# Performance work log

Measured on AMD Instinct MI355X. Metric: run time of the kernel, lower is better.

## Reference

```python
import jax, jax.numpy as jnp
import numpy as np

EMBED_DIM = 1024
NUM_HEADS = 16
HEAD_DIM = EMBED_DIM // NUM_HEADS
ROPE_BASE = 10000.0


def _rope_cos_sin(seq_len, head_dim, dtype):
    # Standard RoPE (ESM-style rotate_half): freqs outer(t, inv_freq), emb = cat(freqs, freqs)
    inv_freq = 1.0 / (ROPE_BASE ** (jnp.arange(0, head_dim, 2, dtype=jnp.float32) / head_dim))
    t = jnp.arange(seq_len, dtype=jnp.float32)
    freqs = jnp.einsum('s,d->sd', t, inv_freq)          # [s, d/2]
    emb = jnp.concatenate([freqs, freqs], axis=-1)      # [s, d]
    return jnp.cos(emb).astype(dtype), jnp.sin(emb).astype(dtype)


def _rotate_half(x):
    x1, x2 = jnp.split(x, 2, axis=-1)
    return jnp.concatenate([-x2, x1], axis=-1)


def _apply_rope(x, cos, sin):
    # x: [b, h, s, d]; cos/sin: [s, d] broadcast over b, h
    return x * cos + _rotate_half(x) * sin


def setup_inputs() -> dict:
    key = jax.random.key(0)
    ks = jax.random.split(key, 5)
    b, s, e = 4, 2048, EMBED_DIM
    scale = 1.0 / np.sqrt(e)
    x = jax.random.normal(ks[0], (b, s, e), dtype=jnp.float32)
    Wqkv = jax.random.normal(ks[1], (e, 3 * e), dtype=jnp.float32) * scale
    bqkv = jnp.zeros((3 * e,), dtype=jnp.float32)
    Wo = jax.random.normal(ks[2], (e, e), dtype=jnp.float32) * scale
    bo = jnp.zeros((e,), dtype=jnp.float32)
    return {"x": x, "Wqkv": Wqkv, "bqkv": bqkv, "Wo": Wo, "bo": bo}


def reference(x, Wqkv, bqkv, Wo, bo):
    b, s, e = x.shape
    h, d = NUM_HEADS, HEAD_DIM
    qkv = jnp.einsum('bse,ef->bsf', x, Wqkv) + bqkv          # [b, s, 3e]
    q, k, v = jnp.split(qkv, 3, axis=-1)
    # b s (h d) -> b h s d
    q = q.reshape(b, s, h, d).transpose(0, 2, 1, 3)
    k = k.reshape(b, s, h, d).transpose(0, 2, 1, 3)
    v = v.reshape(b, s, h, d).transpose(0, 2, 1, 3)
    cos, sin = _rope_cos_sin(s, d, x.dtype)
    q = _apply_rope(q, cos, sin)
    k = _apply_rope(k, cos, sin)
    # scaled dot product attention (no mask, no dropout, non-causal)
    scores = jnp.einsum('bhqd,bhkd->bhqk', q, k) / jnp.asarray(np.sqrt(d), x.dtype)
    attn = jax.nn.softmax(scores, axis=-1)
    out = jnp.einsum('bhqk,bhkd->bhqd', attn, v)             # [b, h, s, d]
    out = out.transpose(0, 2, 1, 3).reshape(b, s, e)         # b h s d -> b s (h d)
    return jnp.einsum('bse,ef->bsf', out, Wo) + bo
```

## Files before the change

kernel.cpp:

```cpp
#include <hip/hip_runtime.h>
#include <stdint.h>
#include <stddef.h>

typedef __bf16 bf16;
typedef __attribute__((ext_vector_type(8))) __bf16 bf16x8;
typedef __attribute__((ext_vector_type(4))) __bf16 bf16x4;
typedef __attribute__((ext_vector_type(4))) float f32x4;
typedef __attribute__((ext_vector_type(4))) float float4v;

#define BATCH 4
#define SEQ   2048
#define EMB   1024
#define NH    16
#define HD    64
#define F3    3072

#define MFMA16(a, b, c) __builtin_amdgcn_mfma_f32_16x16x32_bf16((a), (b), (c), 0, 0, 0)

__device__ __forceinline__ void gload_lds16(const bf16* g, bf16* l) {
  __builtin_amdgcn_global_load_lds(
      (const __attribute__((address_space(1))) uint32_t*)g,
      (__attribute__((address_space(3))) uint32_t*)l, 16, 0, 0);
}

__global__ __launch_bounds__(256) void rope_table(float* __restrict__ cosT,
                                                  float* __restrict__ sinT) {
  int idx = blockIdx.x * 256 + threadIdx.x;
  int pos = idx >> 5, d1 = idx & 31;
  float inv = powf(10000.0f, -(float)(2 * d1) / 64.0f);
  float th = (float)pos * inv;
  cosT[idx] = cosf(th);
  sinT[idx] = sinf(th);
}

__global__ __launch_bounds__(256) void convert_bf16(const float* __restrict__ src,
                                                    bf16* __restrict__ dst, int n4) {
  int i = blockIdx.x * 256 + threadIdx.x;
  if (i >= n4) return;
  float4v v = ((const float4v*)src)[i];
  bf16x4 o;
#pragma unroll
  for (int k = 0; k < 4; ++k) o[k] = (bf16)v[k];
  ((bf16x4*)dst)[i] = o;
}

__global__ __launch_bounds__(256) void transpose_f32_bf16(const float* __restrict__ in,
                                                          bf16* __restrict__ out,
                                                          int R, int C) {
  __shared__ bf16 tile[32][33];
  const int tx = threadIdx.x & 31;
  const int ty = threadIdx.x >> 5;
  const int c0 = blockIdx.x * 32, r0 = blockIdx.y * 32;
#pragma unroll
  for (int kk = 0; kk < 4; ++kk) {
    int r = ty + kk * 8;
    tile[r][tx] = (bf16)in[(size_t)(r0 + r) * C + c0 + tx];
  }
  __syncthreads();
#pragma unroll
  for (int kk = 0; kk < 4; ++kk) {
    int r = ty + kk * 8;
    out[(size_t)(c0 + r) * R + r0 + tx] = tile[tx][r];
  }
}

__global__ __launch_bounds__(256) void qkv_rope_kernel(
    const bf16* __restrict__ x, const bf16* __restrict__ wT,
    const float* __restrict__ bias, bf16* __restrict__ qo, bf16* __restrict__ ko,
    bf16* __restrict__ vo, const float* __restrict__ cosT,
    const float* __restrict__ sinT) {
  __shared__ __align__(16) bf16 As[128 * 32];
  __shared__ __align__(16) bf16 Bs[128 * 32];
  const int tid = threadIdx.x;
  const int w = tid >> 6, lane = tid & 63;
  const int lhi = lane >> 4, llo = lane & 15;
  const int wr = w >> 1, wc = w & 1;
  const int row_a0 = blockIdx.y * 128;
  const int row_b0 = blockIdx.x * 128;

  f32x4 acc[4][4];
#pragma unroll
  for (int i = 0; i < 4; ++i)
#pragma unroll
    for (int j = 0; j < 4; ++j) acc[i][j] = (f32x4){0.f, 0.f, 0.f, 0.f};

  for (int k0 = 0; k0 < EMB; k0 += 32) {
#pragma unroll
    for (int c = 0; c < 2; ++c) {
      int chunk = w * 2 + c;
      int gl = chunk * 64 + lane;
      int row = gl >> 2, kk = (gl & 3) << 3;
      gload_lds16(x + (size_t)(row_a0 + row) * EMB + k0 + kk, &As[chunk * 512]);
      gload_lds16(wT + (size_t)(row_b0 + row) * EMB + k0 + kk, &Bs[chunk * 512]);
    }
    __syncthreads();
    bf16x8 a[4], b[4];
#pragma unroll
    for (int i = 0; i < 4; ++i)
      a[i] = *(const bf16x8*)&As[(wr * 64 + i * 16 + llo) * 32 + lhi * 8];
#pragma unroll
    for (int j = 0; j < 4; ++j)
      b[j] = *(const bf16x8*)&Bs[(wc * 64 + j * 16 + llo) * 32 + lhi * 8];
#pragma unroll
    for (int i = 0; i < 4; ++i)
#pragma unroll
      for (int j = 0; j < 4; ++j) acc[i][j] = MFMA16(a[i], b[j], acc[i][j]);
    __syncthreads();
  }

  const int f0 = row_b0 + wc * 64;
  const int part = f0 >> 10;
  const int hh = (f0 & 1023) >> 6;
  const int m_base = row_a0 + wr * 64;

  float bvals[4];
#pragma unroll
  for (int j = 0; j < 4; ++j) bvals[j] = bias[f0 + j * 16 + llo];

  if (part == 2) {
#pragma unroll
    for (int i = 0; i < 4; ++i) {
      int m0 = m_base + i * 16 + lhi * 4;
      int bb = m0 >> 11, pos0 = m0 & 2047;
#pragma unroll
      for (int j = 0; j < 4; ++j) {
        int dd = j * 16 + llo;
        bf16x4 pk;
#pragma unroll
        for (int r = 0; r < 4; ++r) pk[r] = (bf16)(acc[i][j][r] + bvals[j]);
        *(bf16x4*)(vo + ((size_t)(bb * NH + hh) * HD + dd) * SEQ + pos0) = pk;
      }
    }
  } else {
    bf16* dst = (part == 0) ? qo : ko;
    const float qs = (part == 0) ? 0.125f : 1.0f;
#pragma unroll
    for (int i = 0; i < 4; ++i) {
#pragma unroll
      for (int r = 0; r < 4; ++r) {
        int m = m_base + i * 16 + lhi * 4 + r;
        int bb = m >> 11, pos = m & 2047;
        size_t base = ((size_t)(bb * NH + hh) * SEQ + pos) * HD;
#pragma unroll
        for (int j = 0; j < 2; ++j) {
          int d1 = j * 16 + llo;
          float x1 = acc[i][j][r] + bvals[j];
          float x2 = acc[i][j + 2][r] + bvals[j + 2];
          float cth = cosT[pos * 32 + d1];
          float sth = sinT[pos * 32 + d1];
          dst[base + d1] = (bf16)((x1 * cth - x2 * sth) * qs);
          dst[base + d1 + 32] = (bf16)((x2 * cth + x1 * sth) * qs);
        }
      }
    }
  }
}

__global__ __launch_bounds__(256) void attn_kernel(const bf16* __restrict__ q,
                                                   const bf16* __restrict__ k,
                                                   const bf16* __restrict__ vT,
                                                   bf16* __restrict__ o) {
  __shared__ __align__(16) bf16 smem[24576];
  bf16* Qs = smem;

  const int tid = threadIdx.x, w = tid >> 6, lane = tid & 63;
  const int lhi = lane >> 4, llo = lane & 15;
  const int l7 = llo & 7;
  const int bidx = blockIdx.x;
  const int vblk = (bidx & 7) * 128 + (bidx >> 3);
  const int qt = vblk & 15, bh = vblk >> 4;
  const bf16* qbase = q + (size_t)bh * SEQ * HD + qt * 128 * HD;
  const bf16* kbase = k + (size_t)bh * SEQ * HD;
  const bf16* vbase = vT + (size_t)bh * HD * SEQ;
  bf16* Pw = smem + w * 2048;

  const int rowc = lane >> 3;
  const int sw8 = (lane & 7) ^ rowc;

#pragma unroll
  for (int c = 0; c < 4; ++c) {
    int chunk = w * 4 + c;
    int row = chunk * 8 + rowc;
    gload_lds16(qbase + (size_t)row * HD + sw8 * 8, &Qs[chunk * 512]);
  }
#pragma unroll
  for (int c = 0; c < 2; ++c) {
    int chunk = w * 2 + c;
    int row = chunk * 8 + rowc;
    gload_lds16(kbase + (size_t)row * HD + sw8 * 8, &smem[8192 + chunk * 512]);
    gload_lds16(vbase + (size_t)row * SEQ + sw8 * 8, &smem[16384 + chunk * 512]);
  }
  __syncthreads();

  bf16x8 qf[2][2];
#pragma unroll
  for (int i = 0; i < 2; ++i)
#pragma unroll
    for (int kc = 0; kc < 2; ++kc)
      qf[i][kc] = *(const bf16x8*)&Qs[(w * 32 + i * 16 + llo) * 64 +
                                      (((kc * 4 + lhi) ^ l7) * 8)];
  __syncthreads();

  float rsum[2][4];
  f32x4 oacc[2][4];
#pragma unroll
  for (int i = 0; i < 2; ++i)
#pragma unroll
    for (int r = 0; r < 4; ++r) rsum[i][r] = 0.f;
#pragma unroll
  for (int i = 0; i < 2; ++i)
#pragma unroll
    for (int j = 0; j < 4; ++j) oacc[i][j] = (f32x4){0.f, 0.f, 0.f, 0.f};

  for (int kb = 0; kb < 32; ++kb) {
    bf16* Kc = smem + 8192 + (kb & 1) * 4096;
    bf16* Vc = smem + 16384 + (kb & 1) * 4096;
    if (kb < 31) {
      bf16* Kn = smem + 8192 + ((kb + 1) & 1) * 4096;
      bf16* Vn = smem + 16384 + ((kb + 1) & 1) * 4096;
      int kpos = (kb + 1) * 64;
#pragma unroll
      for (int c = 0; c < 2; ++c) {
        int chunk = w * 2 + c;
        int row = chunk * 8 + rowc;
        gload_lds16(kbase + (size_t)(kpos + row) * HD + sw8 * 8, &Kn[chunk * 512]);
        gload_lds16(vbase + (size_t)row * SEQ + kpos + sw8 * 8, &Vn[chunk * 512]);
      }
    }
    f32x4 sacc[2][4];
#pragma unroll
    for (int i = 0; i < 2; ++i)
#pragma unroll
      for (int jn = 0; jn < 4; ++jn) sacc[i][jn] = (f32x4){0.f, 0.f, 0.f, 0.f};
#pragma unroll
    for (int kc = 0; kc < 2; ++kc) {
      bf16x8 bfr[4];
#pragma unroll
      for (int jn = 0; jn < 4; ++jn)
        bfr[jn] = *(const bf16x8*)&Kc[(jn * 16 + llo) * 64 +
                                      (((kc * 4 + lhi) ^ l7) * 8)];
#pragma unroll
      for (int i = 0; i < 2; ++i)
#pragma unroll
        for (int jn = 0; jn < 4; ++jn)
          sacc[i][jn] = MFMA16(qf[i][kc], bfr[jn], sacc[i][jn]);
    }
#pragma unroll
    for (int i = 0; i < 2; ++i) {
#pragma unroll
      for (int r = 0; r < 4; ++r) {
        int qrow = i * 16 + lhi * 4 + r;
        int qb = qrow * 64, q7 = qrow & 7;
        float acc = 0.f;
#pragma unroll
        for (int jn = 0; jn < 4; ++jn) {
          float p = __expf(sacc[i][jn][r]);
          Pw[qb + (((jn * 2 + (llo >> 3)) ^ q7) * 8) + l7] = (bf16)p;
          acc += p;
        }
        rsum[i][r] += acc;
      }
    }
#pragma unroll
    for (int kc = 0; kc < 2; ++kc) {
      bf16x8 af[2], bv[4];
      int xg = ((kc * 4 + lhi) ^ l7) * 8;
#pragma unroll
      for (int i = 0; i < 2; ++i)
        af[i] = *(const bf16x8*)&Pw[(i * 16 + llo) * 64 + xg];
#pragma unroll
      for (int jd = 0; jd < 4; ++jd)
        bv[jd] = *(const bf16x8*)&Vc[(jd * 16 + llo) * 64 + xg];
#pragma unroll
      for (int i = 0; i < 2; ++i)
#pragma unroll
        for (int jd = 0; jd < 4; ++jd) oacc[i][jd] = MFMA16(af[i], bv[jd], oacc[i][jd]);
    }
    __syncthreads();
  }

  const int bb = bh >> 4, hh = bh & 15;
#pragma unroll
  for (int i = 0; i < 2; ++i) {
#pragma unroll
    for (int r = 0; r < 4; ++r) {
      float t = rsum[i][r];
      t += __shfl_xor(t, 1);
      t += __shfl_xor(t, 2);
      t += __shfl_xor(t, 4);
      t += __shfl_xor(t, 8);
      float inv = 1.0f / t;
      int pos = qt * 128 + w * 32 + i * 16 + lhi * 4 + r;
      size_t base = ((size_t)bb * SEQ + pos) * EMB + hh * HD;
#pragma unroll
      for (int jd = 0; jd < 4; ++jd)
        o[base + jd * 16 + llo] = (bf16)(oacc[i][jd][r] * inv);
    }
  }
}

__global__ __launch_bounds__(256) void outproj_kernel(const bf16* __restrict__ a_in,
                                                      const bf16* __restrict__ wT,
                                                      const float* __restrict__ bo,
                                                      float* __restrict__ out) {
  __shared__ __align__(16) bf16 As[128 * 32];
  __shared__ __align__(16) bf16 Bs[128 * 32];
  const int tid = threadIdx.x;
  const int w = tid >> 6, lane = tid & 63;
  const int lhi = lane >> 4, llo = lane & 15;
  const int wr = w >> 1, wc = w & 1;
  const int row_a0 = blockIdx.y * 128;
  const int row_b0 = blockIdx.x * 128;

  f32x4 acc[4][4];
#pragma unroll
  for (int i = 0; i < 4; ++i)
#pragma unroll
    for (int j = 0; j < 4; ++j) acc[i][j] = (f32x4){0.f, 0.f, 0.f, 0.f};

  for (int k0 = 0; k0 < EMB; k0 += 32) {
#pragma unroll
    for (int c = 0; c < 2; ++c) {
      int chunk = w * 2 + c;
      int gl = chunk * 64 + lane;
      int row = gl >> 2, kk = (gl & 3) << 3;
      gload_lds16(a_in + (size_t)(row_a0 + row) * EMB + k0 + kk, &As[chunk * 512]);
      gload_lds16(wT + (size_t)(row_b0 + row) * EMB + k0 + kk, &Bs[chunk * 512]);
    }
    __syncthreads();
    bf16x8 a[4], b[4];
#pragma unroll
    for (int i = 0; i < 4; ++i)
      a[i] = *(const bf16x8*)&As[(wr * 64 + i * 16 + llo) * 32 + lhi * 8];
#pragma unroll
    for (int j = 0; j < 4; ++j)
      b[j] = *(const bf16x8*)&Bs[(wc * 64 + j * 16 + llo) * 32 + lhi * 8];
#pragma unroll
    for (int i = 0; i < 4; ++i)
#pragma unroll
      for (int j = 0; j < 4; ++j) acc[i][j] = MFMA16(a[i], b[j], acc[i][j]);
    __syncthreads();
  }

  const int col0 = row_b0 + wc * 64;
  const int m_base = row_a0 + wr * 64;
  float bvals[4];
#pragma unroll
  for (int j = 0; j < 4; ++j) bvals[j] = bo[col0 + j * 16 + llo];
#pragma unroll
  for (int i = 0; i < 4; ++i) {
#pragma unroll
    for (int r = 0; r < 4; ++r) {
      int m = m_base + i * 16 + lhi * 4 + r;
#pragma unroll
      for (int j = 0; j < 4; ++j)
        out[(size_t)m * EMB + col0 + j * 16 + llo] = acc[i][j][r] + bvals[j];
    }
  }
}

extern "C" void kernel_launch(void* const* d_in, const int* in_sizes, int n_in,
                              void* d_out, int out_size, void* d_ws, size_t ws_size,
                              hipStream_t stream) {
  const float* x_raw = (const float*)d_in[0];
  const float* wqkv_raw = (const float*)d_in[1];
  const float* bqkv = (const float*)d_in[2];
  const float* wo_raw = (const float*)d_in[3];
  const float* bo = (const float*)d_in[4];
  float* out = (float*)d_out;

  char* ws = (char*)d_ws;
  bf16* qw = (bf16*)(ws);
  bf16* kw = (bf16*)(ws + 16777216);
  bf16* vw = (bf16*)(ws + 33554432);
  bf16* wqkvT = (bf16*)(ws + 50331648);
  float* cosT = (float*)(ws + 56623104);
  float* sinT = (float*)(ws + 56885248);
  bf16* ow = (bf16*)(ws + 50331648);
  bf16* woT = (bf16*)(ws);
  bf16* xb = (bf16*)d_out;

  rope_table<<<256, 256, 0, stream>>>(cosT, sinT);
  convert_bf16<<<(BATCH * SEQ * EMB / 4 + 255) / 256, 256, 0, stream>>>(
      x_raw, xb, BATCH * SEQ * EMB / 4);
  transpose_f32_bf16<<<dim3(F3 / 32, EMB / 32), 256, 0, stream>>>(wqkv_raw, wqkvT, EMB, F3);

  qkv_rope_kernel<<<dim3(F3 / 128, (BATCH * SEQ) / 128), 256, 0, stream>>>(
      xb, wqkvT, bqkv, qw, kw, vw, cosT, sinT);
  attn_kernel<<<dim3(BATCH * NH * (SEQ / 128)), 256, 0, stream>>>(qw, kw, vw, ow);

  transpose_f32_bf16<<<dim3(EMB / 32, EMB / 32), 256, 0, stream>>>(wo_raw, woT, EMB, EMB);
  outproj_kernel<<<dim3(EMB / 128, (BATCH * SEQ) / 128), 256, 0, stream>>>(
      ow, woT, bo, out);
}
```

Before: 309.0 us.

## Widen attention blocks to 256 queries, split K/V loads, transpose score MFMA

The attention kernel now uses 512 threads (8 waves) covering 256 query rows per block, so each K/V tile staged in LDS is shared by twice as many query rows, halving K/V global traffic. Waves 0-3 load K and waves 4-7 load V instead of every wave loading both. The score MFMA is computed as K·Q^T, so each lane holds four consecutive keys for one query. P is then written as packed bf16x4 stores, and the row sum reduces with two shuffles plus a broadcast. The trade-offs are a larger LDS footprint (64 KB per block) and half as many blocks, which may lower occupancy and tail utilisation.

```diff
diff --git a/kernel.cpp b/kernel.cpp
--- a/kernel.cpp
+++ b/kernel.cpp
@@ -156,20 +156,20 @@
   }
 }
 
-__global__ __launch_bounds__(256) void attn_kernel(const bf16* __restrict__ q,
+__global__ __launch_bounds__(512) void attn_kernel(const bf16* __restrict__ q,
                                                    const bf16* __restrict__ k,
                                                    const bf16* __restrict__ vT,
                                                    bf16* __restrict__ o) {
-  __shared__ __align__(16) bf16 smem[24576];
+  __shared__ __align__(16) bf16 smem[32768];
   bf16* Qs = smem;
 
   const int tid = threadIdx.x, w = tid >> 6, lane = tid & 63;
   const int lhi = lane >> 4, llo = lane & 15;
   const int l7 = llo & 7;
   const int bidx = blockIdx.x;
-  const int vblk = (bidx & 7) * 128 + (bidx >> 3);
-  const int qt = vblk & 15, bh = vblk >> 4;
-  const bf16* qbase = q + (size_t)bh * SEQ * HD + qt * 128 * HD;
+  const int vblk = (bidx & 7) * 64 + (bidx >> 3);
+  const int qt = vblk & 7, bh = vblk >> 3;
+  const bf16* qbase = q + (size_t)bh * SEQ * HD + qt * 256 * HD;
   const bf16* kbase = k + (size_t)bh * SEQ * HD;
   const bf16* vbase = vT + (size_t)bh * HD * SEQ;
   bf16* Pw = smem + w * 2048;
@@ -183,12 +183,20 @@
     int row = chunk * 8 + rowc;
     gload_lds16(qbase + (size_t)row * HD + sw8 * 8, &Qs[chunk * 512]);
   }
-#pragma unroll
-  for (int c = 0; c < 2; ++c) {
-    int chunk = w * 2 + c;
-    int row = chunk * 8 + rowc;
-    gload_lds16(kbase + (size_t)row * HD + sw8 * 8, &smem[8192 + chunk * 512]);
-    gload_lds16(vbase + (size_t)row * SEQ + sw8 * 8, &smem[16384 + chunk * 512]);
+  if (w < 4) {
+#pragma unroll
+    for (int c = 0; c < 2; ++c) {
+      int chunk = w * 2 + c;
+      int row = chunk * 8 + rowc;
+      gload_lds16(kbase + (size_t)row * HD + sw8 * 8, &smem[16384 + chunk * 512]);
+    }
+  } else {
+#pragma unroll
+    for (int c = 0; c < 2; ++c) {
+      int chunk = (w - 4) * 2 + c;
+      int row = chunk * 8 + rowc;
+      gload_lds16(vbase + (size_t)row * SEQ + sw8 * 8, &smem[24576 + chunk * 512]);
+    }
   }
   __syncthreads();
 
@@ -201,73 +209,79 @@
                                       (((kc * 4 + lhi) ^ l7) * 8)];
   __syncthreads();
 
-  float rsum[2][4];
+  float rsum[2] = {0.f, 0.f};
   f32x4 oacc[2][4];
 #pragma unroll
   for (int i = 0; i < 2; ++i)
 #pragma unroll
-    for (int r = 0; r < 4; ++r) rsum[i][r] = 0.f;
-#pragma unroll
-  for (int i = 0; i < 2; ++i)
-#pragma unroll
     for (int j = 0; j < 4; ++j) oacc[i][j] = (f32x4){0.f, 0.f, 0.f, 0.f};
 
   for (int kb = 0; kb < 32; ++kb) {
-    bf16* Kc = smem + 8192 + (kb & 1) * 4096;
-    bf16* Vc = smem + 16384 + (kb & 1) * 4096;
+    bf16* Kc = smem + 16384 + (kb & 1) * 4096;
+    bf16* Vc = smem + 24576 + (kb & 1) * 4096;
     if (kb < 31) {
-      bf16* Kn = smem + 8192 + ((kb + 1) & 1) * 4096;
-      bf16* Vn = smem + 16384 + ((kb + 1) & 1) * 4096;
       int kpos = (kb + 1) * 64;
-#pragma unroll
-      for (int c = 0; c < 2; ++c) {
-        int chunk = w * 2 + c;
-        int row = chunk * 8 + rowc;
-        gload_lds16(kbase + (size_t)(kpos + row) * HD + sw8 * 8, &Kn[chunk * 512]);
-        gload_lds16(vbase + (size_t)row * SEQ + kpos + sw8 * 8, &Vn[chunk * 512]);
+      if (w < 4) {
+        bf16* Kn = smem + 16384 + ((kb + 1) & 1) * 4096;
+#pragma unroll
+        for (int c = 0; c < 2; ++c) {
+          int chunk = w * 2 + c;
+          int row = chunk * 8 + rowc;
+          gload_lds16(kbase + (size_t)(kpos + row) * HD + sw8 * 8, &Kn[chunk * 512]);
+        }
+      } else {
+        bf16* Vn = smem + 24576 + ((kb + 1) & 1) * 4096;
+#pragma unroll
+        for (int c = 0; c < 2; ++c) {
+          int chunk = (w - 4) * 2 + c;
+          int row = chunk * 8 + rowc;
+          gload_lds16(vbase + (size_t)row * SEQ + kpos + sw8 * 8, &Vn[chunk * 512]);
+        }
       }
     }
-    f32x4 sacc[2][4];
-#pragma unroll
-    for (int i = 0; i < 2; ++i)
-#pragma unroll
-      for (int jn = 0; jn < 4; ++jn) sacc[i][jn] = (f32x4){0.f, 0.f, 0.f, 0.f};
+    f32x4 st[4][2];
+#pragma unroll
+    for (int tt = 0; tt < 4; ++tt)
+#pragma unroll
+      for (int i = 0; i < 2; ++i) st[tt][i] = (f32x4){0.f, 0.f, 0.f, 0.f};
 #pragma unroll
     for (int kc = 0; kc < 2; ++kc) {
-      bf16x8 bfr[4];
-#pragma unroll
-      for (int jn = 0; jn < 4; ++jn)
-        bfr[jn] = *(const bf16x8*)&Kc[(jn * 16 + llo) * 64 +
+      bf16x8 kfr[4];
+#pragma unroll
+      for (int tt = 0; tt < 4; ++tt)
+        kfr[tt] = *(const bf16x8*)&Kc[(tt * 16 + llo) * 64 +
                                       (((kc * 4 + lhi) ^ l7) * 8)];
 #pragma unroll
-      for (int i = 0; i < 2; ++i)
-#pragma unroll
-        for (int jn = 0; jn < 4; ++jn)
-          sacc[i][jn] = MFMA16(qf[i][kc], bfr[jn], sacc[i][jn]);
-    }
-#pragma unroll
-    for (int i = 0; i < 2; ++i) {
-#pragma unroll
-      for (int r = 0; r < 4; ++r) {
-        int qrow = i * 16 + lhi * 4 + r;
-        int qb = qrow * 64, q7 = qrow & 7;
-        float acc = 0.f;
-#pragma unroll
-        for (int jn = 0; jn < 4; ++jn) {
-          float p = __expf(sacc[i][jn][r]);
-          Pw[qb + (((jn * 2 + (llo >> 3)) ^ q7) * 8) + l7] = (bf16)p;
-          acc += p;
+      for (int tt = 0; tt < 4; ++tt)
+#pragma unroll
+        for (int i = 0; i < 2; ++i)
+          st[tt][i] = MFMA16(kfr[tt], qf[i][kc], st[tt][i]);
+    }
+#pragma unroll
+    for (int tt = 0; tt < 4; ++tt) {
+#pragma unroll
+      for (int i = 0; i < 2; ++i) {
+        bf16x4 pk;
+        float a = 0.f;
+#pragma unroll
+        for (int r = 0; r < 4; ++r) {
+          float p = __expf(st[tt][i][r]);
+          pk[r] = (bf16)p;
+          a += p;
         }
-        rsum[i][r] += acc;
+        rsum[i] += a;
+        int gi = (tt * 4 + lhi) ^ (l7 << 1);
+        *(bf16x4*)&Pw[(i * 16 + llo) * 64 + gi * 4] = pk;
       }
     }
 #pragma unroll
     for (int kc = 0; kc < 2; ++kc) {
       bf16x8 af[2], bv[4];
       int xg = ((kc * 4 + lhi) ^ l7) * 8;
+      int pg = ((kc * 8 + lhi * 2) ^ (l7 << 1)) * 4;
 #pragma unroll
       for (int i = 0; i < 2; ++i)
-        af[i] = *(const bf16x8*)&Pw[(i * 16 + llo) * 64 + xg];
+        af[i] = *(const bf16x8*)&Pw[(i * 16 + llo) * 64 + pg];
 #pragma unroll
       for (int jd = 0; jd < 4; ++jd)
         bv[jd] = *(const bf16x8*)&Vc[(jd * 16 + llo) * 64 + xg];
@@ -282,15 +296,14 @@
   const int bb = bh >> 4, hh = bh & 15;
 #pragma unroll
   for (int i = 0; i < 2; ++i) {
+    float t = rsum[i];
+    t += __shfl_xor(t, 16);
+    t += __shfl_xor(t, 32);
 #pragma unroll
     for (int r = 0; r < 4; ++r) {
-      float t = rsum[i][r];
-      t += __shfl_xor(t, 1);
-      t += __shfl_xor(t, 2);
-      t += __shfl_xor(t, 4);
-      t += __shfl_xor(t, 8);
-      float inv = 1.0f / t;
-      int pos = qt * 128 + w * 32 + i * 16 + lhi * 4 + r;
+      float l = __shfl(t, lhi * 4 + r);
+      float inv = 1.0f / l;
+      int pos = qt * 256 + w * 32 + i * 16 + lhi * 4 + r;
       size_t base = ((size_t)bb * SEQ + pos) * EMB + hh * HD;
 #pragma unroll
       for (int jd = 0; jd < 4; ++jd)
@@ -387,7 +400,7 @@
 
   qkv_rope_kernel<<<dim3(F3 / 128, (BATCH * SEQ) / 128), 256, 0, stream>>>(
       xb, wqkvT, bqkv, qw, kw, vw, cosT, sinT);
-  attn_kernel<<<dim3(BATCH * NH * (SEQ / 128)), 256, 0, stream>>>(qw, kw, vw, ow);
+  attn_kernel<<<dim3(BATCH * NH * (SEQ / 256)), 512, 0, stream>>>(qw, kw, vw, ow);
 
   transpose_f32_bf16<<<dim3(EMB / 32, EMB / 32), 256, 0, stream>>>(wo_raw, woT, EMB, EMB);
   outproj_kernel<<<dim3(EMB / 128, (BATCH * SEQ) / 128), 256, 0, stream>>>(
```

Result: faster. 292.0 us (-5.5%).
